# Optimization experiments

Hardware: AMD Instinct MI355X
Metric: run time of the kernel (lower is better)

Reference implementation:

```python
import jax, jax.numpy as jnp
import numpy as np

VOCAB = 32000
HIDDEN = 1024


def setup_inputs() -> dict:
    key = jax.random.key(0)
    ks = jax.random.split(key, 8)
    B, S = 2, 2048
    x = jax.random.randint(ks[0], (B, S), 0, VOCAB)
    scale = 0.02
    emb = jax.random.normal(ks[1], (VOCAB, HIDDEN), jnp.float32) * scale
    pos_emb = jax.random.normal(ks[2], (VOCAB, HIDDEN), jnp.float32) * scale
    Wk = jax.random.normal(ks[3], (HIDDEN, HIDDEN), jnp.float32) * scale
    Wq = jax.random.normal(ks[4], (HIDDEN, HIDDEN), jnp.float32) * scale
    Wv = jax.random.normal(ks[5], (HIDDEN, HIDDEN), jnp.float32) * scale
    Wo = jax.random.normal(ks[6], (HIDDEN, VOCAB), jnp.float32) * scale
    bo = jnp.zeros((VOCAB,), jnp.float32)
    return {"x": x, "emb": emb, "pos_emb": pos_emb, "Wk": Wk, "Wq": Wq, "Wv": Wv, "Wo": Wo, "bo": bo}


def reference(x, emb, pos_emb, Wk, Wq, Wv, Wo, bo):
    B, S = x.shape
    # token + positional embedding
    h = emb[x] + pos_emb[jnp.arange(S)][None, :, :]  # [B,S,H]
    q = jnp.einsum("bsh,hd->bsd", h, Wq)
    k = jnp.einsum("bsh,hd->bsd", h, Wk)
    v = jnp.einsum("bsh,hd->bsd", h, Wv)
    scores = jnp.einsum("bsd,btd->bst", q, k) / jnp.sqrt(jnp.float32(HIDDEN))
    causal = jnp.tril(jnp.ones((S, S), bool))  # [S,S]
    scores = jnp.where(causal[None], scores, jnp.finfo(scores.dtype).min)
    attn = jax.nn.softmax(scores, axis=-1)
    attn = attn * causal[None].astype(attn.dtype)  # explicit tril * z as in source
    z = jnp.einsum("bst,btd->bsd", attn, v) + h  # residual
    out = jnp.einsum("bsd,dv->bsv", z, Wo) + bo  # [B,S,VOCAB]
    return out
```

## Files before the change

kernel.cpp:

```cpp
#include <hip/hip_runtime.h>

typedef unsigned short u16;
typedef __bf16 bf16x8 __attribute__((ext_vector_type(8)));
typedef float f32x4 __attribute__((ext_vector_type(4)));

#define GAS __attribute__((address_space(1)))
#define LAS __attribute__((address_space(3)))

__device__ __forceinline__ void async_copy16(const void* g, void* l) {
    __builtin_amdgcn_global_load_lds((GAS void*)g, (LAS void*)l, 16, 0, 0);
}

__device__ __forceinline__ u16 f2bf(float f) {
    unsigned int u = __float_as_uint(f);
    u = (u + 0x7fffu + ((u >> 16) & 1u)) >> 16;
    return (u16)u;
}
__device__ __forceinline__ float bf2f(u16 h) {
    return __uint_as_float(((unsigned int)h) << 16);
}

__device__ __forceinline__ void store_val(float* p, float v) { *p = v; }
__device__ __forceinline__ void store_val(u16* p, float v) { *p = f2bf(v); }

template <typename OutT, bool ADD_RES, bool ADD_BIAS>
__global__ void gemm_bt(const u16* __restrict__ A, long sA,
                        const u16* __restrict__ Bt, long sB,
                        OutT* __restrict__ C, long sC,
                        const u16* __restrict__ Res,
                        const float* __restrict__ bias,
                        int K, int lda, int ldb, int ldc, float alpha) {
    constexpr int BM = 128, BN = 128, BK = 32;
    __shared__ u16 As[BM * BK];
    __shared__ u16 Bs[BN * BK];

    const int tid  = threadIdx.x;
    const int lane = tid & 63;
    const int wid  = tid >> 6;
    const long bm  = (long)blockIdx.y * BM;
    const long bn  = (long)blockIdx.x * BN;
    const long z   = blockIdx.z;

    A  += z * sA;
    Bt += z * sB;
    C  += z * sC;
    const u16* R = Res + z * sC;

    const int srow = tid >> 2;
    const int scol = (tid & 3) * 8;
    const u16* ag0 = A + (bm + srow) * (long)lda + scol;
    const u16* ag1 = A + (bm + srow + 64) * (long)lda + scol;
    const u16* bg0 = Bt + (bn + srow) * (long)ldb + scol;
    const u16* bg1 = Bt + (bn + srow + 64) * (long)ldb + scol;
    u16* al0 = &As[srow * BK + scol];
    u16* al1 = &As[(srow + 64) * BK + scol];
    u16* bl0 = &Bs[srow * BK + scol];
    u16* bl1 = &Bs[(srow + 64) * BK + scol];

    const int wm   = (wid & 1) * 64;
    const int wn   = (wid >> 1) * 64;
    const int frow = lane & 15;
    const int fk   = (lane >> 4) * 8;

    f32x4 acc[4][4];
#pragma unroll
    for (int i = 0; i < 4; i++)
#pragma unroll
        for (int j = 0; j < 4; j++) acc[i][j] = f32x4{0.f, 0.f, 0.f, 0.f};

    for (int k0 = 0; k0 < K; k0 += BK) {
        async_copy16(ag0 + k0, al0);
        async_copy16(ag1 + k0, al1);
        async_copy16(bg0 + k0, bl0);
        async_copy16(bg1 + k0, bl1);
        __syncthreads();

        bf16x8 af[4], bfv[4];
#pragma unroll
        for (int i = 0; i < 4; i++)
            af[i] = *(const bf16x8*)&As[(wm + i * 16 + frow) * BK + fk];
#pragma unroll
        for (int j = 0; j < 4; j++)
            bfv[j] = *(const bf16x8*)&Bs[(wn + j * 16 + frow) * BK + fk];
#pragma unroll
        for (int i = 0; i < 4; i++)
#pragma unroll
            for (int j = 0; j < 4; j++)
                acc[i][j] = __builtin_amdgcn_mfma_f32_16x16x32_bf16(
                    af[i], bfv[j], acc[i][j], 0, 0, 0);
        __syncthreads();
    }

    const int r0 = (lane >> 4) * 4;
#pragma unroll
    for (int i = 0; i < 4; i++) {
#pragma unroll
        for (int j = 0; j < 4; j++) {
            const long col = bn + wn + j * 16 + frow;
            float badd = 0.f;
            if constexpr (ADD_BIAS) badd = bias[col];
#pragma unroll
            for (int r = 0; r < 4; r++) {
                const long row = bm + wm + i * 16 + r0 + r;
                float v = acc[i][j][r] * alpha + badd;
                if constexpr (ADD_RES) v += bf2f(R[row * (long)ldc + col]);
                store_val(&C[row * (long)ldc + col], v);
            }
        }
    }
}

__global__ void transpose_f32_bf16(const float* __restrict__ in, u16* __restrict__ out,
                                   int R, int C) {
    __shared__ float tile[32][33];
    const int bx = blockIdx.x * 32;
    const int by = blockIdx.y * 32;
    const int tx = threadIdx.x, ty = threadIdx.y;
#pragma unroll
    for (int i = 0; i < 32; i += 8)
        tile[ty + i][tx] = in[(long)(by + ty + i) * C + (bx + tx)];
    __syncthreads();
#pragma unroll
    for (int i = 0; i < 32; i += 8)
        out[(long)(bx + ty + i) * R + (by + tx)] = f2bf(tile[tx][ty + i]);
}

__global__ void embed_kernel(const int* __restrict__ x, const float* __restrict__ emb,
                             const float* __restrict__ pos, u16* __restrict__ h, int S) {
    const int row = blockIdx.x;
    const int s   = row % S;
    const int tok = x[row];
    const int t   = threadIdx.x;
    const float4 e = ((const float4*)(emb + (long)tok * 1024))[t];
    const float4 p = ((const float4*)(pos + (long)s * 1024))[t];
    unsigned int lo = (unsigned)f2bf(e.x + p.x) | ((unsigned)f2bf(e.y + p.y) << 16);
    unsigned int hi = (unsigned)f2bf(e.z + p.z) | ((unsigned)f2bf(e.w + p.w) << 16);
    ((uint2*)(h + (long)row * 1024))[t] = make_uint2(lo, hi);
}

__global__ void softmax_causal(const float* __restrict__ sc, u16* __restrict__ attn,
                               int S, float scale) {
    const int row = blockIdx.x;
    const int s   = row % S;
    const int n   = s + 1;
    const float* r = sc + (long)row * S;
    u16* o = attn + (long)row * S;
    const int tid = threadIdx.x, lane = tid & 63, wid = tid >> 6;
    __shared__ float red[4];

    float mx = -3.0e38f;
    for (int i = tid; i < n; i += 256) mx = fmaxf(mx, r[i]);
#pragma unroll
    for (int off = 32; off; off >>= 1) mx = fmaxf(mx, __shfl_xor(mx, off, 64));
    if (lane == 0) red[wid] = mx;
    __syncthreads();
    mx = fmaxf(fmaxf(red[0], red[1]), fmaxf(red[2], red[3])) * scale;

    float sum = 0.f;
    for (int i = tid; i < n; i += 256) sum += __expf(r[i] * scale - mx);
#pragma unroll
    for (int off = 32; off; off >>= 1) sum += __shfl_xor(sum, off, 64);
    __syncthreads();
    if (lane == 0) red[wid] = sum;
    __syncthreads();
    const float inv = 1.f / (red[0] + red[1] + red[2] + red[3]);

    for (int i = tid; i < n; i += 256) o[i] = f2bf(__expf(r[i] * scale - mx) * inv);
    for (int i = n + tid; i < S; i += 256) o[i] = 0;
}

extern "C" void kernel_launch(void* const* d_in, const int* in_sizes, int n_in,
                              void* d_out, int out_size, void* d_ws, size_t ws_size,
                              hipStream_t stream) {
    const int B = 2, S = 2048, H = 1024, V = 32000;
    const int* x     = (const int*)d_in[0];
    const float* emb = (const float*)d_in[1];
    const float* pos = (const float*)d_in[2];
    const float* Wk  = (const float*)d_in[3];
    const float* Wq  = (const float*)d_in[4];
    const float* Wv  = (const float*)d_in[5];
    const float* Wo  = (const float*)d_in[6];
    const float* bo  = (const float*)d_in[7];
    float* out = (float*)d_out;

    char* ws = (char*)d_ws;
    u16* h_bf   = (u16*)(ws + 0);
    u16* WqT    = (u16*)(ws + 8388608);
    u16* WkT    = (u16*)(ws + 10485760);
    u16* WvT    = (u16*)(ws + 12582912);
    u16* WoT    = (u16*)(ws + 14680064);
    u16* q_bf   = (u16*)(ws + 80216064);
    u16* k_bf   = (u16*)(ws + 88604672);
    u16* vT_bf  = (u16*)(ws + 96993280);
    float* scor = (float*)(ws + 105381888);
    u16* attn   = (u16*)(ws + 138936320);
    u16* z_bf   = (u16*)(ws + 155713536);

    dim3 ttb(32, 8);
    transpose_f32_bf16<<<dim3(32, 32), ttb, 0, stream>>>(Wq, WqT, H, H);
    transpose_f32_bf16<<<dim3(32, 32), ttb, 0, stream>>>(Wk, WkT, H, H);
    transpose_f32_bf16<<<dim3(32, 32), ttb, 0, stream>>>(Wv, WvT, H, H);
    transpose_f32_bf16<<<dim3(V / 32, 32), ttb, 0, stream>>>(Wo, WoT, H, V);

    embed_kernel<<<B * S, 256, 0, stream>>>(x, emb, pos, h_bf, S);

    gemm_bt<u16, false, false><<<dim3(8, 32, 1), 256, 0, stream>>>(
        h_bf, 0, WqT, 0, q_bf, 0, nullptr, nullptr, H, H, H, H, 1.0f);
    gemm_bt<u16, false, false><<<dim3(8, 32, 1), 256, 0, stream>>>(
        h_bf, 0, WkT, 0, k_bf, 0, nullptr, nullptr, H, H, H, H, 1.0f);
    gemm_bt<u16, false, false><<<dim3(32, 8, 1), 256, 0, stream>>>(
        WvT, 0, h_bf, 0, vT_bf, 0, nullptr, nullptr, H, H, H, B * S, 1.0f);

    gemm_bt<float, false, false><<<dim3(16, 16, B), 256, 0, stream>>>(
        q_bf, (long)S * H, k_bf, (long)S * H, scor, (long)S * S,
        nullptr, nullptr, H, H, H, S, 1.0f);

    softmax_causal<<<B * S, 256, 0, stream>>>(scor, attn, S, 0.03125f);

    gemm_bt<u16, true, false><<<dim3(8, 16, B), 256, 0, stream>>>(
        attn, (long)S * S, vT_bf, (long)S, z_bf, (long)S * H,
        h_bf, nullptr, S, S, B * S, H, 1.0f);

    gemm_bt<float, false, true><<<dim3(V / 128, 32, 1), 256, 0, stream>>>(
        z_bf, 0, WoT, 0, out, 0, nullptr, bo, H, H, H, V, 1.0f);
}
```

Before: 1.250 ms.

## Add 256x256 double-buffered swizzled GEMM for vocab output projection

Replaces the 128x128 GEMM used for the large output projection with a new 256x256-tile kernel using 512 threads, 128KB dynamic LDS, and double-buffered async global-to-LDS loads. It also applies XOR-swizzled LDS layouts, interleaves MFMA phases with prefetch under s_setprio, remaps workgroups across XCDs, and writes the output with nontemporal stores. The goal is more data reuse per tile, compute overlapped with loads, and fewer LDS bank conflicts in the dominant GEMM. In exchange the kernel carries more register and LDS pressure and depends on hand-written waitcnt ordering.

Result: faster. 1.156 ms (-7.6%).

```diff
diff --git a/kernel.cpp b/kernel.cpp
--- a/kernel.cpp
+++ b/kernel.cpp
@@ -105,6 +105,122 @@
                 float v = acc[i][j][r] * alpha + badd;
                 if constexpr (ADD_RES) v += bf2f(R[row * (long)ldc + col]);
                 store_val(&C[row * (long)ldc + col], v);
+            }
+        }
+    }
+}
+
+#define GPHASE(buf, kk, VM, ...)                                              \
+    {                                                                         \
+        const u16* pa = lA + (((buf) * 4 + (kk)) << 13);                      \
+        const u16* pb = lB + (((buf) * 4 + 2 + (kk)) << 13);                  \
+        bf16x8 af[8], bv[4];                                                  \
+        _Pragma("unroll") for (int i_ = 0; i_ < 8; i_++)                      \
+            af[i_] = *(const bf16x8*)(pa + i_ * 512);                         \
+        _Pragma("unroll") for (int j_ = 0; j_ < 4; j_++)                      \
+            bv[j_] = *(const bf16x8*)(pb + j_ * 512);                         \
+        __VA_ARGS__;                                                          \
+        asm volatile("" ::: "memory");                                        \
+        __builtin_amdgcn_s_barrier();                                         \
+        __builtin_amdgcn_s_setprio(1);                                        \
+        _Pragma("unroll") for (int i_ = 0; i_ < 8; i_++)                      \
+            _Pragma("unroll") for (int j_ = 0; j_ < 4; j_++)                  \
+                acc[i_][j_] = __builtin_amdgcn_mfma_f32_16x16x32_bf16(        \
+                    af[i_], bv[j_], acc[i_][j_], 0, 0, 0);                    \
+        __builtin_amdgcn_s_setprio(0);                                        \
+        VM;                                                                   \
+        asm volatile("" ::: "memory");                                        \
+        __builtin_amdgcn_s_barrier();                                         \
+        asm volatile("" ::: "memory");                                        \
+    }
+
+template <bool ADD_BIAS>
+__global__ __launch_bounds__(512, 2)
+void gemm256_bt(const u16* __restrict__ A, const u16* __restrict__ Bt,
+                float* __restrict__ C, const float* __restrict__ bias,
+                int K, int lda, int ldb, int ldc, int tilesN) {
+    extern __shared__ u16 lds[];
+
+    const int tid  = threadIdx.x;
+    const int lane = tid & 63;
+    const int wid  = tid >> 6;
+    const int wr   = wid >> 2;
+    const int wc   = wid & 3;
+
+    const int bid = (int)blockIdx.x;
+    const int nwg = (int)gridDim.x;
+    int wgid = bid;
+    if ((nwg & 7) == 0) wgid = (bid & 7) * (nwg >> 3) + (bid >> 3);
+    const long bm = (long)(wgid / tilesN) * 256;
+    const long bn = (long)(wgid % tilesN) * 256;
+
+    const int srow  = tid >> 2;
+    const int schk  = ((tid & 3) ^ ((tid >> 3) & 3)) << 3;
+    const u16* Ag = A + (bm + srow) * (long)lda + schk;
+    const u16* Bg = Bt + (bn + srow) * (long)ldb + schk;
+    u16* ldsw = lds + tid * 8;
+
+    auto stage2 = [&](int buf, int kk, int t) {
+        const long ko = (long)t * 64 + kk * 32;
+        const u16* a  = Ag + ko;
+        const u16* b  = Bg + ko;
+        u16* dA = ldsw + (((buf * 4) + kk) << 13);
+        u16* dB = ldsw + (((buf * 4) + 2 + kk) << 13);
+        async_copy16(a, dA);
+        async_copy16(a + (long)lda * 128, dA + 4096);
+        async_copy16(b, dB);
+        async_copy16(b + (long)ldb * 128, dB + 4096);
+    };
+
+    const int fr    = lane & 15;
+    const int cSwzE = (((lane >> 4) ^ ((lane >> 1) & 3)) << 3);
+    const u16* lA = lds + (wr * 128 + fr) * 32 + cSwzE;
+    const u16* lB = lds + (wc * 64 + fr) * 32 + cSwzE;
+
+    f32x4 acc[8][4];
+#pragma unroll
+    for (int i = 0; i < 8; i++)
+#pragma unroll
+        for (int j = 0; j < 4; j++) acc[i][j] = f32x4{0.f, 0.f, 0.f, 0.f};
+
+    const int NT = K >> 6;
+
+    stage2(0, 0, 0);
+    stage2(0, 1, 0);
+    stage2(1, 0, 1);
+    asm volatile("s_waitcnt vmcnt(4)" ::: "memory");
+    __builtin_amdgcn_s_barrier();
+    asm volatile("" ::: "memory");
+
+    int t = 0;
+    for (; t < NT - 2; ++t) {
+        const int buf = t & 1;
+        GPHASE(buf, 0, , stage2(buf ^ 1, 1, t + 1));
+        GPHASE(buf, 1, asm volatile("s_waitcnt vmcnt(4)" ::: "memory"),
+               stage2(buf, 0, t + 2));
+    }
+    {
+        const int buf = t & 1;
+        GPHASE(buf, 0, , stage2(buf ^ 1, 1, t + 1));
+        GPHASE(buf, 1, asm volatile("s_waitcnt vmcnt(0)" ::: "memory"), );
+        const int buf2 = buf ^ 1;
+        GPHASE(buf2, 0, , );
+        GPHASE(buf2, 1, , );
+    }
+
+    const int r0 = (lane >> 4) * 4;
+#pragma unroll
+    for (int j = 0; j < 4; j++) {
+        const long col = bn + wc * 64 + j * 16 + fr;
+        float badd = 0.f;
+        if constexpr (ADD_BIAS) badd = bias[col];
+#pragma unroll
+        for (int i = 0; i < 8; i++) {
+#pragma unroll
+            for (int r = 0; r < 4; r++) {
+                const long row = bm + wr * 128 + i * 16 + r0 + r;
+                __builtin_nontemporal_store(acc[i][j][r] + badd,
+                                            &C[row * (long)ldc + col]);
             }
         }
     }
@@ -196,6 +312,13 @@
     u16* attn   = (u16*)(ws + 138936320);
     u16* z_bf   = (u16*)(ws + 155713536);
 
+    static int lds_opt_in = 0;
+    if (!lds_opt_in) {
+        hipFuncSetAttribute((const void*)gemm256_bt<true>,
+                            hipFuncAttributeMaxDynamicSharedMemorySize, 131072);
+        lds_opt_in = 1;
+    }
+
     dim3 ttb(32, 8);
     transpose_f32_bf16<<<dim3(32, 32), ttb, 0, stream>>>(Wq, WqT, H, H);
     transpose_f32_bf16<<<dim3(32, 32), ttb, 0, stream>>>(Wk, WkT, H, H);
@@ -221,6 +344,6 @@
         attn, (long)S * S, vT_bf, (long)S, z_bf, (long)S * H,
         h_bf, nullptr, S, S, B * S, H, 1.0f);
 
-    gemm_bt<float, false, true><<<dim3(V / 128, 32, 1), 256, 0, stream>>>(
-        z_bf, 0, WoT, 0, out, 0, nullptr, bo, H, H, H, V, 1.0f);
-}
+    gemm256_bt<true><<<dim3((V / 256) * (4096 / 256), 1, 1), 512, 131072, stream>>>(
+        z_bf, WoT, out, bo, H, H, H, V, V / 256);
+}
```
